# Kernel tuning notes

Hardware: AMD Instinct MI355X
Metric: run time of the kernel (lower is better)

Reference implementation:

```python
import jax, jax.numpy as jnp
import numpy as np

B, L, D, DI = 4, 4096, 2048, 256
LN_EPS = 1e-5


def setup_inputs() -> dict:
    key = jax.random.key(0)
    ks = jax.random.split(key, 5)
    x = jax.random.normal(ks[0], (B, L, D), jnp.float32)
    # xavier-ish scale for in/out projections, std=0.01 for scan projections (as in _init_weights)
    W_in = jax.random.normal(ks[1], (D, DI), jnp.float32) * np.float32(1.0 / np.sqrt(D))
    W_fwd = jax.random.normal(ks[2], (DI, 2 * DI), jnp.float32) * np.float32(0.01)
    W_bwd = jax.random.normal(ks[3], (DI, 2 * DI), jnp.float32) * np.float32(0.01)
    W_out = jax.random.normal(ks[4], (2 * DI, D), jnp.float32) * np.float32(1.0 / np.sqrt(2 * DI))
    gamma = jnp.ones((D,), jnp.float32)
    beta = jnp.zeros((D,), jnp.float32)
    return {"x": x, "W_in": W_in, "W_fwd": W_fwd, "W_bwd": W_bwd, "W_out": W_out, "gamma": gamma, "beta": beta}


def _scan_dir(z, Wp):
    """Gated linear recurrence h_t = delta_t * h_{t-1} + gate_t, with delta/gate from one GEMM.
    z: [B, L, d]; Wp: [d, 2d] -> returns [B, L, d]."""
    d = z.shape[-1]
    o = jnp.einsum("bld,de->ble", z, Wp)          # [B, L, 2d]
    delta = jax.nn.sigmoid(o[..., :d])             # [B, L, d]
    gate = o[..., d:] * z                          # [B, L, d]

    def step(h, dg):
        dlt, g = dg
        h = h * dlt + g
        return h, h

    h0 = jnp.zeros_like(z[:, 0])                   # [B, d]
    _, hs = jax.lax.scan(step, h0, (jnp.swapaxes(delta, 0, 1), jnp.swapaxes(gate, 0, 1)))
    return jnp.swapaxes(hs, 0, 1)                  # [B, L, d]


def reference(x, W_in, W_fwd, W_bwd, W_out, gamma, beta):
    z = jnp.einsum("bld,de->ble", x, W_in)         # [B, L, DI]
    h_fwd = _scan_dir(z, W_fwd)
    h_bwd = _scan_dir(z[:, ::-1], W_bwd)[:, ::-1]
    out = jnp.einsum("ble,ed->bld", jnp.concatenate([h_fwd, h_bwd], axis=-1), W_out)
    y = out + x                                    # residual
    mu = jnp.mean(y, axis=-1, keepdims=True)
    var = jnp.var(y, axis=-1, keepdims=True)
    return (y - mu) * jax.lax.rsqrt(var + LN_EPS) * gamma + beta
```

## Files before the change

kernel.cpp:

```cpp
#include <hip/hip_runtime.h>
#include <hip/hip_bf16.h>

using bf16 = __hip_bfloat16;
typedef float float4v __attribute__((ext_vector_type(4)));
typedef __bf16 bf16x8 __attribute__((ext_vector_type(8)));
typedef unsigned short ushort4v __attribute__((ext_vector_type(4)));
typedef unsigned short ushort8v __attribute__((ext_vector_type(8)));

#define B_  4
#define L_  4096
#define D_  2048
#define DI_ 256
#define M_  (B_*L_)
#define NC  64
#define LC  (L_/NC)

__device__ inline float bf2f(bf16 x) { return __bfloat162float(x); }
__device__ inline bf16  f2bf(float x) { return __float2bfloat16(x); }

__device__ inline void store4bf(bf16* p, float4v v) {
    ushort4v u;
#pragma unroll
    for (int i = 0; i < 4; i++) {
        bf16 h = f2bf(v[i]);
        u[i] = *(unsigned short*)&h;
    }
    *(ushort4v*)p = u;
}

__device__ inline float4v load4bf(const bf16* p) {
    ushort4v u = *(const ushort4v*)p;
    float4v v;
#pragma unroll
    for (int i = 0; i < 4; i++) v[i] = __uint_as_float(((unsigned)u[i]) << 16);
    return v;
}

__device__ inline ushort8v cvt8(float4v a, float4v b) {
    ushort8v u;
#pragma unroll
    for (int i = 0; i < 4; i++) {
        bf16 h0 = f2bf(a[i]); u[i]     = *(unsigned short*)&h0;
        bf16 h1 = f2bf(b[i]); u[i + 4] = *(unsigned short*)&h1;
    }
    return u;
}

__device__ __forceinline__ void gload_lds16(const bf16* g, bf16* l) {
    __builtin_amdgcn_global_load_lds((const __attribute__((address_space(1))) void*)(g),
                                     (__attribute__((address_space(3))) void*)(l),
                                     16, 0, 0);
}

__global__ void transpose_cvt(const float* __restrict__ in, bf16* __restrict__ out,
                              int R, int C, int obase) {
    int idx = blockIdx.x * 256 + threadIdx.x;
    if (idx < R * C) {
        int r = idx / C, c = idx - r * C;
        out[(size_t)(c + obase) * R + r] = f2bf(in[idx]);
    }
}

#define BK 32

template<int TBM, int TBN, int EPI, bool AF32>
__global__ __launch_bounds__(256) void gemm_bt(const void* __restrict__ Av,
                                               const bf16* __restrict__ BT,
                                               int K, int N,
                                               bf16* __restrict__ o0, bf16* __restrict__ o1,
                                               bf16* __restrict__ o2, bf16* __restrict__ o3,
                                               const bf16* __restrict__ auxb,
                                               const float* __restrict__ auxf) {
    constexpr int MI  = TBM / 32, NI = TBN / 32, AP = TBM / 64, BP = TBN / 64;
    constexpr int ASZ = TBM * 32, BSZ = TBN * 32;
    __shared__ __align__(16) bf16 As[2 * ASZ];
    __shared__ __align__(16) bf16 Bs[2 * BSZ];
    const int tid  = threadIdx.x;
    const int bm   = blockIdx.x, bn = blockIdx.y;
    const int lane = tid & 63, wave = tid >> 6;
    const int wm   = (wave >> 1) * (TBM / 2), wn = (wave & 1) * (TBN / 2);
    const int l15  = lane & 15, quad = lane >> 4;
    const int rsub  = lane >> 2;
    const int kslot = (lane & 3) ^ ((lane >> 3) & 3);
    const int sq    = quad ^ ((l15 >> 1) & 3);
    const int sr    = tid >> 2, scs = tid & 3;
    const int swslot = scs ^ ((sr >> 1) & 3);

    float4v acc[MI][NI] = {};
    const float* Af = (const float*)Av;
    const bf16*  Ab = (const bf16*)Av;
    float4v fa[AP][2];

    auto stage_a = [&](int buf, int kk) {
#pragma unroll
        for (int p = 0; p < AP; p++) {
            int rbase = wave * (TBM / 4) + p * 16;
            gload_lds16(Ab + (size_t)(bm * TBM + rbase + rsub) * K + kk + kslot * 8,
                        As + buf * ASZ + rbase * 32 + lane * 8);
        }
    };
    auto stage_b = [&](int buf, int kk) {
#pragma unroll
        for (int p = 0; p < BP; p++) {
            int rbase = wave * (TBN / 4) + p * 16;
            gload_lds16(BT + (size_t)(bn * TBN + rbase + rsub) * K + kk + kslot * 8,
                        Bs + buf * BSZ + rbase * 32 + lane * 8);
        }
    };
    auto load_a_f32 = [&](int kk) {
#pragma unroll
        for (int p = 0; p < AP; p++) {
            const float* src = Af + (size_t)(bm * TBM + p * 64 + sr) * K + kk + scs * 8;
            fa[p][0] = *(const float4v*)src;
            fa[p][1] = *(const float4v*)(src + 4);
        }
    };
    auto write_a_f32 = [&](int buf) {
#pragma unroll
        for (int p = 0; p < AP; p++)
            *(ushort8v*)(As + buf * ASZ + (p * 64 + sr) * 32 + swslot * 8)
                = cvt8(fa[p][0], fa[p][1]);
    };
    auto compute = [&](int buf) {
        bf16x8 af[MI], bfr[NI];
#pragma unroll
        for (int mi = 0; mi < MI; mi++)
            af[mi] = *(const bf16x8*)(As + buf * ASZ + (wm + mi * 16 + l15) * 32 + sq * 8);
#pragma unroll
        for (int ni = 0; ni < NI; ni++)
            bfr[ni] = *(const bf16x8*)(Bs + buf * BSZ + (wn + ni * 16 + l15) * 32 + sq * 8);
#pragma unroll
        for (int mi = 0; mi < MI; mi++)
#pragma unroll
            for (int ni = 0; ni < NI; ni++)
                acc[mi][ni] = __builtin_amdgcn_mfma_f32_16x16x32_bf16(
                    bfr[ni], af[mi], acc[mi][ni], 0, 0, 0);
    };

    if constexpr (AF32) load_a_f32(0); else stage_a(0, 0);
    stage_b(0, 0);
    if constexpr (AF32) write_a_f32(0);
    __syncthreads();

    const int nt = K / BK;
    int cur = 0;
    for (int t = 0; t < nt; t++) {
        if (t + 1 < nt) {
            if constexpr (AF32) load_a_f32((t + 1) * BK);
            else                stage_a(cur ^ 1, (t + 1) * BK);
            stage_b(cur ^ 1, (t + 1) * BK);
        }
        compute(cur);
        if (t + 1 < nt) {
            if constexpr (AF32) write_a_f32(cur ^ 1);
            __syncthreads();
        }
        cur ^= 1;
    }

#pragma unroll
    for (int mi = 0; mi < MI; mi++) {
#pragma unroll
        for (int ni = 0; ni < NI; ni++) {
            int row = bm * TBM + wm + mi * 16 + l15;
            int col = bn * TBN + wn + ni * 16 + quad * 4;
            float4v v = acc[mi][ni];
            if (EPI == 0) {
                store4bf(o0 + (size_t)row * N + col, v);
            } else if (EPI == 1) {
                int sel = col >> 8, d = col & 255;
                bf16* dst = (sel == 0) ? o0 : (sel == 1) ? o1 : (sel == 2) ? o2 : o3;
                if (sel & 1) {
                    float4v z4 = load4bf(auxb + (size_t)row * DI_ + d);
#pragma unroll
                    for (int i = 0; i < 4; i++) v[i] *= z4[i];
                } else {
#pragma unroll
                    for (int i = 0; i < 4; i++) v[i] = 1.f / (1.f + __expf(-v[i]));
                }
                store4bf(dst + (size_t)row * DI_ + d, v);
            } else {
                float4v r = *(const float4v*)(auxf + (size_t)row * N + col);
#pragma unroll
                for (int i = 0; i < 4; i++) v[i] += r[i];
                store4bf(o0 + (size_t)row * N + col, v);
            }
        }
    }
}

__global__ __launch_bounds__(256) void scan_agg(const bf16* __restrict__ del_f,
                                                const bf16* __restrict__ gat_f,
                                                const bf16* __restrict__ del_b,
                                                const bf16* __restrict__ gat_b,
                                                float* __restrict__ aggA,
                                                float* __restrict__ aggB) {
    int c = blockIdx.x, b = blockIdx.y, dir = blockIdx.z, d = threadIdx.x;
    const bf16* delta = dir ? del_b : del_f;
    const bf16* gate  = dir ? gat_b : gat_f;
    float Ap = 1.f, h = 0.f;
    for (int i = 0; i < LC; i++) {
        int t = dir ? (L_ - 1 - (c * LC + i)) : (c * LC + i);
        size_t base = ((size_t)(b * L_ + t)) * DI_ + d;
        float dlt = bf2f(delta[base]);
        float g   = bf2f(gate[base]);
        Ap *= dlt;
        h = h * dlt + g;
    }
    size_t idx = (((size_t)dir * B_ + b) * NC + c) * DI_ + d;
    aggA[idx] = Ap;
    aggB[idx] = h;
}

__global__ void scan_mid(const float* __restrict__ aggA, const float* __restrict__ aggB,
                         float* __restrict__ Hin) {
    int b = blockIdx.x, dir = blockIdx.y, d = threadIdx.x;
    float h = 0.f;
    for (int c = 0; c < NC; c++) {
        size_t idx = (((size_t)dir * B_ + b) * NC + c) * DI_ + d;
        Hin[idx] = h;
        h = aggA[idx] * h + aggB[idx];
    }
}

__global__ __launch_bounds__(256) void scan_fix(const bf16* __restrict__ del_f,
                                                const bf16* __restrict__ gat_f,
                                                const bf16* __restrict__ del_b,
                                                const bf16* __restrict__ gat_b,
                                                const float* __restrict__ Hin,
                                                bf16* __restrict__ hcat) {
    int c = blockIdx.x, b = blockIdx.y, dir = blockIdx.z, d = threadIdx.x;
    const bf16* delta = dir ? del_b : del_f;
    const bf16* gate  = dir ? gat_b : gat_f;
    float h = Hin[(((size_t)dir * B_ + b) * NC + c) * DI_ + d];
    int colbase = dir * DI_;
    for (int i = 0; i < LC; i++) {
        int t = dir ? (L_ - 1 - (c * LC + i)) : (c * LC + i);
        size_t base = ((size_t)(b * L_ + t)) * DI_ + d;
        float dlt = bf2f(delta[base]);
        float g   = bf2f(gate[base]);
        h = h * dlt + g;
        hcat[((size_t)(b * L_ + t)) * (2 * DI_) + colbase + d] = f2bf(h);
    }
}

__global__ __launch_bounds__(256) void ln_kernel(const bf16* __restrict__ y,
                                                 const float* __restrict__ gamma,
                                                 const float* __restrict__ beta,
                                                 float* __restrict__ outp) {
    __shared__ float ss[4], ssq[4];
    int row = blockIdx.x, tid = threadIdx.x;
    size_t base = (size_t)row * D_ + tid * 8;
    uint4 raw = *(const uint4*)(y + base);
    const unsigned short* u = (const unsigned short*)&raw;
    float v[8];
    float s = 0.f, sq = 0.f;
#pragma unroll
    for (int i = 0; i < 8; i++) {
        v[i] = __uint_as_float(((unsigned)u[i]) << 16);
        s += v[i];
        sq += v[i] * v[i];
    }
    for (int o = 32; o > 0; o >>= 1) { s += __shfl_down(s, o); sq += __shfl_down(sq, o); }
    if ((tid & 63) == 0) { ss[tid >> 6] = s; ssq[tid >> 6] = sq; }
    __syncthreads();
    float S  = ss[0] + ss[1] + ss[2] + ss[3];
    float SQ = ssq[0] + ssq[1] + ssq[2] + ssq[3];
    float mean = S * (1.f / D_);
    float var  = SQ * (1.f / D_) - mean * mean;
    float rstd = rsqrtf(var + 1e-5f);
    float4v g0 = *(const float4v*)(gamma + tid * 8);
    float4v g1 = *(const float4v*)(gamma + tid * 8 + 4);
    float4v b0 = *(const float4v*)(beta + tid * 8);
    float4v b1 = *(const float4v*)(beta + tid * 8 + 4);
    float4v r0, r1;
#pragma unroll
    for (int i = 0; i < 4; i++) {
        r0[i] = (v[i] - mean) * rstd * g0[i] + b0[i];
        r1[i] = (v[i + 4] - mean) * rstd * g1[i] + b1[i];
    }
    *(float4v*)(outp + base)     = r0;
    *(float4v*)(outp + base + 4) = r1;
}

extern "C" void kernel_launch(void* const* d_in, const int* in_sizes, int n_in,
                              void* d_out, int out_size, void* d_ws, size_t ws_size,
                              hipStream_t stream) {
    (void)in_sizes; (void)n_in; (void)out_size; (void)ws_size;
    const float* x     = (const float*)d_in[0];
    const float* W_in  = (const float*)d_in[1];
    const float* W_fwd = (const float*)d_in[2];
    const float* W_bwd = (const float*)d_in[3];
    const float* W_out = (const float*)d_in[4];
    const float* gamma = (const float*)d_in[5];
    const float* beta  = (const float*)d_in[6];
    float* out = (float*)d_out;

    char* ws = (char*)d_ws;
    size_t off = 0;
    auto alloc = [&](size_t bytes) -> char* {
        char* p = ws + off;
        off += (bytes + 255) & ~(size_t)255;
        return p;
    };
    bf16*  WinT   = (bf16*)alloc((size_t)DI_ * D_ * 2);
    bf16*  WpT    = (bf16*)alloc((size_t)1024 * DI_ * 2);
    bf16*  WoutT  = (bf16*)alloc((size_t)D_ * 2 * DI_ * 2);
    bf16*  z      = (bf16*)alloc((size_t)M_ * DI_ * 2);
    bf16*  del_f  = (bf16*)alloc((size_t)M_ * DI_ * 2);
    bf16*  gat_f  = (bf16*)alloc((size_t)M_ * DI_ * 2);
    bf16*  del_b  = (bf16*)alloc((size_t)M_ * DI_ * 2);
    bf16*  gat_b  = (bf16*)alloc((size_t)M_ * DI_ * 2);
    bf16*  hcat   = (bf16*)alloc((size_t)M_ * 2 * DI_ * 2);
    bf16*  ybuf   = (bf16*)alloc((size_t)M_ * D_ * 2);
    float* aggA   = (float*)alloc((size_t)2 * B_ * NC * DI_ * 4);
    float* aggB   = (float*)alloc((size_t)2 * B_ * NC * DI_ * 4);
    float* Hin    = (float*)alloc((size_t)2 * B_ * NC * DI_ * 4);

    transpose_cvt<<<(D_ * DI_ + 255) / 256, 256, 0, stream>>>(W_in, WinT, D_, DI_, 0);
    transpose_cvt<<<(DI_ * 2 * DI_ + 255) / 256, 256, 0, stream>>>(W_fwd, WpT, DI_, 2 * DI_, 0);
    transpose_cvt<<<(DI_ * 2 * DI_ + 255) / 256, 256, 0, stream>>>(W_bwd, WpT, DI_, 2 * DI_, 2 * DI_);
    transpose_cvt<<<(2 * DI_ * D_ + 255) / 256, 256, 0, stream>>>(W_out, WoutT, 2 * DI_, D_, 0);

    gemm_bt<128, 64, 0, true><<<dim3(M_ / 128, DI_ / 64), 256, 0, stream>>>(
        x, WinT, D_, DI_, z, nullptr, nullptr, nullptr, nullptr, nullptr);

    gemm_bt<128, 128, 1, false><<<dim3(M_ / 128, 1024 / 128), 256, 0, stream>>>(
        z, WpT, DI_, 1024, del_f, gat_f, del_b, gat_b, z, nullptr);

    scan_agg<<<dim3(NC, B_, 2), DI_, 0, stream>>>(del_f, gat_f, del_b, gat_b, aggA, aggB);
    scan_mid<<<dim3(B_, 2), DI_, 0, stream>>>(aggA, aggB, Hin);
    scan_fix<<<dim3(NC, B_, 2), DI_, 0, stream>>>(del_f, gat_f, del_b, gat_b, Hin, hcat);

    gemm_bt<128, 128, 2, false><<<dim3(M_ / 128, D_ / 128), 256, 0, stream>>>(
        hcat, WoutT, 2 * DI_, D_, ybuf, nullptr, nullptr, nullptr, nullptr, x);

    ln_kernel<<<M_, 256, 0, stream>>>(ybuf, gamma, beta, out);
}
```

Baseline: 440.6 us.

## Deepen GEMM prefetch to two stages with explicit vmcnt waits and wider input tile

Reworks the GEMM main loop so global loads run two K-tiles ahead, using explicit s_waitcnt vmcnt counts and raw barriers instead of __syncthreads. The fp32-A path now double-buffers in registers. MFMA sections are wrapped in s_setprio so the math gets scheduling priority. The input projection GEMM switches to a 64x256 tile so each block covers all 256 output columns and the fp32 x tile is read only once. This adds register pressure and relies on hand-counted vmcnt values being correct.

Result: no change. 446.2 us (+1.3%).

```diff
diff --git a/kernel.cpp b/kernel.cpp
--- a/kernel.cpp
+++ b/kernel.cpp
@@ -50,6 +50,18 @@
     __builtin_amdgcn_global_load_lds((const __attribute__((address_space(1))) void*)(g),
                                      (__attribute__((address_space(3))) void*)(l),
                                      16, 0, 0);
+}
+
+template<int N> __device__ __forceinline__ void vmwait() {
+    asm volatile("s_waitcnt vmcnt(%0)" :: "n"(N) : "memory");
+}
+template<int N> __device__ __forceinline__ void vmwait_lgkm0() {
+    asm volatile("s_waitcnt vmcnt(%0) lgkmcnt(0)" :: "n"(N) : "memory");
+}
+__device__ __forceinline__ void bar() {
+    asm volatile("" ::: "memory");
+    __builtin_amdgcn_s_barrier();
+    asm volatile("" ::: "memory");
 }
 
 __global__ void transpose_cvt(const float* __restrict__ in, bf16* __restrict__ out,
@@ -73,6 +85,8 @@
                                                const float* __restrict__ auxf) {
     constexpr int MI  = TBM / 32, NI = TBN / 32, AP = TBM / 64, BP = TBN / 64;
     constexpr int ASZ = TBM * 32, BSZ = TBN * 32;
+    constexpr int TOPW = AF32 ? (2 * AP + BP) : (AP + BP);
+    constexpr int MIDW = 2 * AP + 2 * BP;
     __shared__ __align__(16) bf16 As[2 * ASZ];
     __shared__ __align__(16) bf16 Bs[2 * BSZ];
     const int tid  = threadIdx.x;
@@ -89,7 +103,7 @@
     float4v acc[MI][NI] = {};
     const float* Af = (const float*)Av;
     const bf16*  Ab = (const bf16*)Av;
-    float4v fa[AP][2];
+    float4v fa0[AP][2], fa1[AP][2];
 
     auto stage_a = [&](int buf, int kk) {
 #pragma unroll
@@ -107,7 +121,7 @@
                         Bs + buf * BSZ + rbase * 32 + lane * 8);
         }
     };
-    auto load_a_f32 = [&](int kk) {
+    auto load_a_f32 = [&](float4v (&fa)[AP][2], int kk) {
 #pragma unroll
         for (int p = 0; p < AP; p++) {
             const float* src = Af + (size_t)(bm * TBM + p * 64 + sr) * K + kk + scs * 8;
@@ -115,7 +129,7 @@
             fa[p][1] = *(const float4v*)(src + 4);
         }
     };
-    auto write_a_f32 = [&](int buf) {
+    auto write_a_f32 = [&](float4v (&fa)[AP][2], int buf) {
 #pragma unroll
         for (int p = 0; p < AP; p++)
             *(ushort8v*)(As + buf * ASZ + (p * 64 + sr) * 32 + swslot * 8)
@@ -129,33 +143,57 @@
 #pragma unroll
         for (int ni = 0; ni < NI; ni++)
             bfr[ni] = *(const bf16x8*)(Bs + buf * BSZ + (wn + ni * 16 + l15) * 32 + sq * 8);
+        __builtin_amdgcn_s_setprio(1);
 #pragma unroll
         for (int mi = 0; mi < MI; mi++)
 #pragma unroll
             for (int ni = 0; ni < NI; ni++)
                 acc[mi][ni] = __builtin_amdgcn_mfma_f32_16x16x32_bf16(
                     bfr[ni], af[mi], acc[mi][ni], 0, 0, 0);
-    };
-
-    if constexpr (AF32) load_a_f32(0); else stage_a(0, 0);
-    stage_b(0, 0);
-    if constexpr (AF32) write_a_f32(0);
-    __syncthreads();
+        __builtin_amdgcn_s_setprio(0);
+    };
 
     const int nt = K / BK;
-    int cur = 0;
-    for (int t = 0; t < nt; t++) {
-        if (t + 1 < nt) {
-            if constexpr (AF32) load_a_f32((t + 1) * BK);
-            else                stage_a(cur ^ 1, (t + 1) * BK);
-            stage_b(cur ^ 1, (t + 1) * BK);
-        }
-        compute(cur);
-        if (t + 1 < nt) {
-            if constexpr (AF32) write_a_f32(cur ^ 1);
-            __syncthreads();
-        }
-        cur ^= 1;
+
+    if constexpr (AF32) {
+        load_a_f32(fa0, 0);
+        stage_b(0, 0);
+        load_a_f32(fa1, BK);
+        stage_b(1, BK);
+        vmwait<MIDW>();
+        write_a_f32(fa0, 0);
+
+        auto body = [&](int t, int buf, float4v (&fT)[AP][2], float4v (&fT1)[AP][2]) {
+            if (t == nt - 1) vmwait_lgkm0<0>(); else vmwait_lgkm0<TOPW>();
+            bar();
+            compute(buf);
+            bar();
+            if (t + 2 < nt) {
+                load_a_f32(fT, (t + 2) * BK);
+                stage_b(buf, (t + 2) * BK);
+                vmwait<MIDW>();
+            } else if (t + 1 < nt) {
+                vmwait<BP>();
+            }
+            if (t + 1 < nt) write_a_f32(fT1, buf ^ 1);
+        };
+        for (int t = 0; t < nt; t += 2) {
+            body(t, 0, fa0, fa1);
+            body(t + 1, 1, fa1, fa0);
+        }
+    } else {
+        stage_a(0, 0);  stage_b(0, 0);
+        stage_a(1, BK); stage_b(1, BK);
+        for (int t = 0; t < nt; t++) {
+            if (t == nt - 1) vmwait<0>(); else vmwait<TOPW>();
+            bar();
+            compute(t & 1);
+            bar();
+            if (t + 2 < nt) {
+                stage_a(t & 1, (t + 2) * BK);
+                stage_b(t & 1, (t + 2) * BK);
+            }
+        }
     }
 
 #pragma unroll
@@ -322,7 +360,7 @@
     transpose_cvt<<<(DI_ * 2 * DI_ + 255) / 256, 256, 0, stream>>>(W_bwd, WpT, DI_, 2 * DI_, 2 * DI_);
     transpose_cvt<<<(2 * DI_ * D_ + 255) / 256, 256, 0, stream>>>(W_out, WoutT, 2 * DI_, D_, 0);
 
-    gemm_bt<128, 64, 0, true><<<dim3(M_ / 128, DI_ / 64), 256, 0, stream>>>(
+    gemm_bt<64, 256, 0, true><<<dim3(M_ / 64, 1), 256, 0, stream>>>(
         x, WinT, D_, DI_, z, nullptr, nullptr, nullptr, nullptr, nullptr);
 
     gemm_bt<128, 128, 1, false><<<dim3(M_ / 128, 1024 / 128), 256, 0, stream>>>(
```
